# Performance work log

Measured on AMD Instinct MI355X. Metric: run time of the kernel, lower is better.

The kernel has to match this reference:

```python
import jax, jax.numpy as jnp
import numpy as np

VOCAB = 32000
H = 1024          # hidden_size + 8
I = 2 * H         # gru input size
SRC = 4096

def setup_inputs() -> dict:
    key = jax.random.key(0)
    ks = jax.random.split(key, 12)
    s = 0.02
    return {
        "word_input": jax.random.randint(ks[0], (1, 1), 0, VOCAB),
        "last_context": jax.random.normal(ks[1], (1, 1, H), jnp.float32),
        "prev_hidden": jax.random.normal(ks[2], (1, 1, H), jnp.float32),
        "encoder_outputs": jax.random.normal(ks[3], (SRC, 1, H), jnp.float32),
        "emb": jax.random.normal(ks[4], (VOCAB, H), jnp.float32) * s,
        "W_ih": jax.random.normal(ks[5], (3 * H, I), jnp.float32) * s,
        "W_hh": jax.random.normal(ks[6], (3 * H, H), jnp.float32) * s,
        "b_ih": jax.random.normal(ks[7], (3 * H,), jnp.float32) * s,
        "b_hh": jax.random.normal(ks[8], (3 * H,), jnp.float32) * s,
        "W_out": jax.random.normal(ks[9], (VOCAB, I), jnp.float32) * s,
        "b_out": jax.random.normal(ks[10], (VOCAB,), jnp.float32) * s,
    }

def reference(word_input, last_context, prev_hidden, encoder_outputs,
              emb, W_ih, W_hh, b_ih, b_hh, W_out, b_out):
    # embedding lookup (dropout is identity in eval)
    x = emb[word_input.reshape(-1)[0]]                # (H,)
    rnn_in = jnp.concatenate([x, last_context[0, 0]])  # (2H,)
    h = prev_hidden[0, 0]                              # (H,)

    # single-step GRU (PyTorch gate order: r, z, n)
    gi = W_ih @ rnn_in + b_ih                          # (3H,)
    gh = W_hh @ h + b_hh                               # (3H,)
    i_r, i_z, i_n = jnp.split(gi, 3)
    h_r, h_z, h_n = jnp.split(gh, 3)
    r = jax.nn.sigmoid(i_r + h_r)
    z = jax.nn.sigmoid(i_z + h_z)
    n = jnp.tanh(i_n + r * h_n)
    h_new = (1.0 - z) * n + z * h                      # (H,)
    current_hidden = h_new.reshape(1, 1, H)

    # Luong dot attention over encoder outputs
    enc = encoder_outputs[:, 0, :]                     # (S, H)
    scores = enc @ h_new                               # (S,)
    attn_weights = jax.nn.softmax(scores).reshape(1, 1, -1)
    attn_context = (attn_weights[0] @ enc).reshape(1, 1, H)

    joined = jnp.concatenate([h_new, attn_context[0, 0]])  # (2H,)
    logits = joined @ W_out.T + b_out                  # (vocab,)
    output = jax.nn.log_softmax(logits).reshape(1, -1)
    return (output, attn_context, current_hidden, attn_weights)
```

## Files before the change

### kernel.cpp

```cpp
#include <hip/hip_runtime.h>
#include <math.h>

#define H      1024
#define I2     2048
#define G3     3072
#define SRC    4096
#define VOCAB  32000

#define OUT_CTX   32000
#define OUT_HID   33024
#define OUT_ATTW  34048

#define WS_GI     0
#define WS_GH     3072
#define WS_HNEW   6144
#define WS_SCORES 7168
#define WS_ATTW   11264
#define WS_CTX    15360
#define WS_LOGITS 16384
#define WS_STATS  48384

__device__ __forceinline__ float wave_reduce_sum(float v) {
    #pragma unroll
    for (int off = 32; off > 0; off >>= 1)
        v += __shfl_down(v, off, 64);
    return v;
}

__device__ __forceinline__ float wave_reduce_max(float v) {
    #pragma unroll
    for (int off = 32; off > 0; off >>= 1)
        v = fmaxf(v, __shfl_down(v, off, 64));
    return v;
}

__global__ void gru_matvec_kernel(const int* __restrict__ word,
                                  const float* __restrict__ last_ctx,
                                  const float* __restrict__ prev_h,
                                  const float* __restrict__ emb,
                                  const float* __restrict__ W_ih,
                                  const float* __restrict__ W_hh,
                                  const float* __restrict__ b_ih,
                                  const float* __restrict__ b_hh,
                                  float* __restrict__ ws) {
    __shared__ float lds[8];
    const int j = blockIdx.x;
    const int tid = threadIdx.x;
    const int w = word[0];
    const float4* emb4 = (const float4*)(emb + (long)w * H);
    const float4* ctx4 = (const float4*)last_ctx;
    const float4* h4   = (const float4*)prev_h;

    const float4* Wi = (const float4*)(W_ih + (long)j * I2);
    float gi = 0.f;
    {
        float4 wv = Wi[tid];
        float4 xv = emb4[tid];
        gi += wv.x*xv.x + wv.y*xv.y + wv.z*xv.z + wv.w*xv.w;
        wv = Wi[tid + 256];
        xv = ctx4[tid];
        gi += wv.x*xv.x + wv.y*xv.y + wv.z*xv.z + wv.w*xv.w;
    }
    const float4* Wh = (const float4*)(W_hh + (long)j * H);
    float gh;
    {
        float4 wv = Wh[tid];
        float4 hv = h4[tid];
        gh = wv.x*hv.x + wv.y*hv.y + wv.z*hv.z + wv.w*hv.w;
    }

    const int lane = tid & 63, wid = tid >> 6;
    gi = wave_reduce_sum(gi);
    gh = wave_reduce_sum(gh);
    if (lane == 0) { lds[wid] = gi; lds[4 + wid] = gh; }
    __syncthreads();
    if (tid == 0) {
        float gis = lds[0] + lds[1] + lds[2] + lds[3];
        float ghs = lds[4] + lds[5] + lds[6] + lds[7];
        ws[WS_GI + j] = gis + b_ih[j];
        ws[WS_GH + j] = ghs + b_hh[j];
    }
}

__global__ void gru_gates_kernel(const float* __restrict__ prev_h,
                                 float* __restrict__ ws,
                                 float* __restrict__ out_hid) {
    const int j = threadIdx.x;
    const float ir = ws[WS_GI + j],        hr = ws[WS_GH + j];
    const float iz = ws[WS_GI + H + j],    hz = ws[WS_GH + H + j];
    const float in_ = ws[WS_GI + 2*H + j], hn = ws[WS_GH + 2*H + j];
    const float r = 1.f / (1.f + expf(-(ir + hr)));
    const float z = 1.f / (1.f + expf(-(iz + hz)));
    const float n = tanhf(in_ + r * hn);
    const float h = prev_h[j];
    const float hnew = (1.f - z) * n + z * h;
    ws[WS_HNEW + j] = hnew;
    out_hid[j] = hnew;
}

__global__ void attn_scores_kernel(const float* __restrict__ enc,
                                   const float* __restrict__ ws_in,
                                   float* __restrict__ ws) {
    __shared__ float lds[4];
    const int s = blockIdx.x, tid = threadIdx.x;
    float4 ev = ((const float4*)(enc + (long)s * H))[tid];
    float4 hv = ((const float4*)(ws_in + WS_HNEW))[tid];
    float d = ev.x*hv.x + ev.y*hv.y + ev.z*hv.z + ev.w*hv.w;
    const int lane = tid & 63, wid = tid >> 6;
    d = wave_reduce_sum(d);
    if (lane == 0) lds[wid] = d;
    __syncthreads();
    if (tid == 0) ws[WS_SCORES + s] = lds[0] + lds[1] + lds[2] + lds[3];
}

__global__ void attn_softmax_kernel(float* __restrict__ ws,
                                    float* __restrict__ out_attw) {
    __shared__ float lds[16];
    __shared__ float s_max, s_sum;
    const int tid = threadIdx.x;
    const int lane = tid & 63, wid = tid >> 6;
    float4 sv = ((const float4*)(ws + WS_SCORES))[tid];
    float m = fmaxf(fmaxf(sv.x, sv.y), fmaxf(sv.z, sv.w));
    m = wave_reduce_max(m);
    if (lane == 0) lds[wid] = m;
    __syncthreads();
    if (tid == 0) {
        float mm = lds[0];
        #pragma unroll
        for (int i = 1; i < 16; ++i) mm = fmaxf(mm, lds[i]);
        s_max = mm;
    }
    __syncthreads();
    const float mx = s_max;
    float4 e;
    e.x = expf(sv.x - mx); e.y = expf(sv.y - mx);
    e.z = expf(sv.z - mx); e.w = expf(sv.w - mx);
    float s = e.x + e.y + e.z + e.w;
    s = wave_reduce_sum(s);
    if (lane == 0) lds[wid] = s;
    __syncthreads();
    if (tid == 0) {
        float t = 0.f;
        #pragma unroll
        for (int i = 0; i < 16; ++i) t += lds[i];
        s_sum = t;
    }
    __syncthreads();
    const float inv = 1.f / s_sum;
    float4 o = make_float4(e.x*inv, e.y*inv, e.z*inv, e.w*inv);
    ((float4*)(ws + WS_ATTW))[tid] = o;
    ((float4*)out_attw)[tid] = o;
    ws[WS_CTX + tid] = 0.f;
}

__global__ void attn_context_kernel(const float* __restrict__ enc,
                                    float* __restrict__ ws) {
    const int tid = threadIdx.x;
    const int s0 = blockIdx.x * 128;
    float4 acc = make_float4(0.f, 0.f, 0.f, 0.f);
    for (int s = s0; s < s0 + 128; ++s) {
        const float wgt = ws[WS_ATTW + s];
        float4 ev = ((const float4*)(enc + (long)s * H))[tid];
        acc.x += wgt * ev.x; acc.y += wgt * ev.y;
        acc.z += wgt * ev.z; acc.w += wgt * ev.w;
    }
    float* ctx = ws + WS_CTX + tid * 4;
    atomicAdd(ctx + 0, acc.x); atomicAdd(ctx + 1, acc.y);
    atomicAdd(ctx + 2, acc.z); atomicAdd(ctx + 3, acc.w);
}

__global__ void out_proj_kernel(const float* __restrict__ W_out,
                                const float* __restrict__ b_out,
                                float* __restrict__ ws,
                                float* __restrict__ out_ctx) {
    const int tid = threadIdx.x;
    const int lane = tid & 63, wid = tid >> 6;
    const int v = blockIdx.x * 4 + wid;
    const float4* Wr = (const float4*)(W_out + (long)v * I2);
    const float4* h4 = (const float4*)(ws + WS_HNEW);
    const float4* c4 = (const float4*)(ws + WS_CTX);
    float acc = 0.f;
    #pragma unroll
    for (int r = 0; r < 8; ++r) {
        const int idx = lane + r * 64;
        float4 wv = Wr[idx];
        float4 jv = (r < 4) ? h4[idx] : c4[idx - 256];
        acc += wv.x*jv.x + wv.y*jv.y + wv.z*jv.z + wv.w*jv.w;
    }
    acc = wave_reduce_sum(acc);
    if (lane == 0) ws[WS_LOGITS + v] = acc + b_out[v];
    if (blockIdx.x == 0) {
        for (int k = tid; k < H; k += 256) out_ctx[k] = ws[WS_CTX + k];
    }
}

__global__ void lse_kernel(float* __restrict__ ws) {
    __shared__ float lds[16];
    __shared__ float s_max;
    const int tid = threadIdx.x;
    const int lane = tid & 63, wid = tid >> 6;
    const float* lg = ws + WS_LOGITS;
    float m = -INFINITY;
    for (int v = tid; v < VOCAB; v += 1024) m = fmaxf(m, lg[v]);
    m = wave_reduce_max(m);
    if (lane == 0) lds[wid] = m;
    __syncthreads();
    if (tid == 0) {
        float mm = lds[0];
        #pragma unroll
        for (int i = 1; i < 16; ++i) mm = fmaxf(mm, lds[i]);
        s_max = mm;
    }
    __syncthreads();
    const float mx = s_max;
    float s = 0.f;
    for (int v = tid; v < VOCAB; v += 1024) s += expf(lg[v] - mx);
    s = wave_reduce_sum(s);
    if (lane == 0) lds[wid] = s;
    __syncthreads();
    if (tid == 0) {
        float t = 0.f;
        #pragma unroll
        for (int i = 0; i < 16; ++i) t += lds[i];
        ws[WS_STATS] = mx + logf(t);
    }
}

__global__ void logsoftmax_write_kernel(const float* __restrict__ ws,
                                        float* __restrict__ out) {
    const int v = blockIdx.x * 256 + threadIdx.x;
    if (v < VOCAB) out[v] = ws[WS_LOGITS + v] - ws[WS_STATS];
}

extern "C" void kernel_launch(void* const* d_in, const int* in_sizes, int n_in,
                              void* d_out, int out_size, void* d_ws, size_t ws_size,
                              hipStream_t stream) {
    const int*   word     = (const int*)  d_in[0];
    const float* last_ctx = (const float*)d_in[1];
    const float* prev_h   = (const float*)d_in[2];
    const float* enc      = (const float*)d_in[3];
    const float* emb      = (const float*)d_in[4];
    const float* W_ih     = (const float*)d_in[5];
    const float* W_hh     = (const float*)d_in[6];
    const float* b_ih     = (const float*)d_in[7];
    const float* b_hh     = (const float*)d_in[8];
    const float* W_out    = (const float*)d_in[9];
    const float* b_out    = (const float*)d_in[10];
    float* out = (float*)d_out;
    float* ws  = (float*)d_ws;

    gru_matvec_kernel<<<G3, 256, 0, stream>>>(word, last_ctx, prev_h, emb,
                                              W_ih, W_hh, b_ih, b_hh, ws);
    gru_gates_kernel<<<1, 1024, 0, stream>>>(prev_h, ws, out + OUT_HID);
    attn_scores_kernel<<<SRC, 256, 0, stream>>>(enc, ws, ws);
    attn_softmax_kernel<<<1, 1024, 0, stream>>>(ws, out + OUT_ATTW);
    attn_context_kernel<<<32, 256, 0, stream>>>(enc, ws);
    out_proj_kernel<<<VOCAB / 4, 256, 0, stream>>>(W_out, b_out, ws, out + OUT_CTX);
    lse_kernel<<<1, 1024, 0, stream>>>(ws);
    logsoftmax_write_kernel<<<(VOCAB + 255) / 256, 256, 0, stream>>>(ws, out);
}
```

Baseline: 475.6 us.

## Fuse attention softmax into context kernel, add nontemporal weight loads, vectorize tails

Merges the single-block attention softmax into the context kernel. Each of 128 blocks recomputes the softmax statistics redundantly and weights its own 32-row slice of encoder outputs, and the context zeroing moves into the gate kernel. Weight matrices are streamed with nontemporal loads. The output projection now does 4 rows per wave, with the joined vector staged in LDS. The LSE and log-softmax write kernels use float4 accesses. This removes one launch and raises parallelism in the context reduction, at the cost of redundant softmax work in every block and more atomics.

```diff
diff --git a/kernel.cpp b/kernel.cpp
--- a/kernel.cpp
+++ b/kernel.cpp
@@ -15,7 +15,6 @@
 #define WS_GH     3072
 #define WS_HNEW   6144
 #define WS_SCORES 7168
-#define WS_ATTW   11264
 #define WS_CTX    15360
 #define WS_LOGITS 16384
 #define WS_STATS  48384
@@ -32,6 +31,13 @@
     for (int off = 32; off > 0; off >>= 1)
         v = fmaxf(v, __shfl_down(v, off, 64));
     return v;
+}
+
+typedef float vfloat4 __attribute__((ext_vector_type(4)));
+
+__device__ __forceinline__ float4 nt_load4(const float4* p) {
+    vfloat4 v = __builtin_nontemporal_load((const vfloat4*)p);
+    return make_float4(v.x, v.y, v.z, v.w);
 }
 
 __global__ void gru_matvec_kernel(const int* __restrict__ word,
@@ -54,17 +60,17 @@
     const float4* Wi = (const float4*)(W_ih + (long)j * I2);
     float gi = 0.f;
     {
-        float4 wv = Wi[tid];
+        float4 wv = nt_load4(&Wi[tid]);
         float4 xv = emb4[tid];
         gi += wv.x*xv.x + wv.y*xv.y + wv.z*xv.z + wv.w*xv.w;
-        wv = Wi[tid + 256];
+        wv = nt_load4(&Wi[tid + 256]);
         xv = ctx4[tid];
         gi += wv.x*xv.x + wv.y*xv.y + wv.z*xv.z + wv.w*xv.w;
     }
     const float4* Wh = (const float4*)(W_hh + (long)j * H);
     float gh;
     {
-        float4 wv = Wh[tid];
+        float4 wv = nt_load4(&Wh[tid]);
         float4 hv = h4[tid];
         gh = wv.x*hv.x + wv.y*hv.y + wv.z*hv.z + wv.w*hv.w;
     }
@@ -96,6 +102,7 @@
     const float hnew = (1.f - z) * n + z * h;
     ws[WS_HNEW + j] = hnew;
     out_hid[j] = hnew;
+    ws[WS_CTX + j] = 0.f;
 }
 
 __global__ void attn_scores_kernel(const float* __restrict__ enc,
@@ -113,53 +120,49 @@
     if (tid == 0) ws[WS_SCORES + s] = lds[0] + lds[1] + lds[2] + lds[3];
 }
 
-__global__ void attn_softmax_kernel(float* __restrict__ ws,
-                                    float* __restrict__ out_attw) {
-    __shared__ float lds[16];
-    __shared__ float s_max, s_sum;
-    const int tid = threadIdx.x;
-    const int lane = tid & 63, wid = tid >> 6;
-    float4 sv = ((const float4*)(ws + WS_SCORES))[tid];
-    float m = fmaxf(fmaxf(sv.x, sv.y), fmaxf(sv.z, sv.w));
+__global__ void attn_fused_kernel(const float* __restrict__ enc,
+                                  float* __restrict__ ws,
+                                  float* __restrict__ out_attw) {
+    __shared__ float s_e[SRC];
+    __shared__ float red[4];
+    __shared__ float s_stat;
+    const int tid = threadIdx.x;
+    const int lane = tid & 63, wid = tid >> 6;
+    const float4* sc4 = (const float4*)(ws + WS_SCORES);
+
+    float4 sv[4];
+    float m = -INFINITY;
+    #pragma unroll
+    for (int i = 0; i < 4; ++i) {
+        sv[i] = sc4[tid + 256 * i];
+        m = fmaxf(m, fmaxf(fmaxf(sv[i].x, sv[i].y), fmaxf(sv[i].z, sv[i].w)));
+    }
     m = wave_reduce_max(m);
-    if (lane == 0) lds[wid] = m;
-    __syncthreads();
-    if (tid == 0) {
-        float mm = lds[0];
-        #pragma unroll
-        for (int i = 1; i < 16; ++i) mm = fmaxf(mm, lds[i]);
-        s_max = mm;
-    }
-    __syncthreads();
-    const float mx = s_max;
-    float4 e;
-    e.x = expf(sv.x - mx); e.y = expf(sv.y - mx);
-    e.z = expf(sv.z - mx); e.w = expf(sv.w - mx);
-    float s = e.x + e.y + e.z + e.w;
-    s = wave_reduce_sum(s);
-    if (lane == 0) lds[wid] = s;
-    __syncthreads();
-    if (tid == 0) {
-        float t = 0.f;
-        #pragma unroll
-        for (int i = 0; i < 16; ++i) t += lds[i];
-        s_sum = t;
-    }
-    __syncthreads();
-    const float inv = 1.f / s_sum;
-    float4 o = make_float4(e.x*inv, e.y*inv, e.z*inv, e.w*inv);
-    ((float4*)(ws + WS_ATTW))[tid] = o;
-    ((float4*)out_attw)[tid] = o;
-    ws[WS_CTX + tid] = 0.f;
-}
-
-__global__ void attn_context_kernel(const float* __restrict__ enc,
-                                    float* __restrict__ ws) {
-    const int tid = threadIdx.x;
-    const int s0 = blockIdx.x * 128;
+    if (lane == 0) red[wid] = m;
+    __syncthreads();
+    if (tid == 0) s_stat = fmaxf(fmaxf(red[0], red[1]), fmaxf(red[2], red[3]));
+    __syncthreads();
+    const float mx = s_stat;
+    float sum = 0.f;
+    #pragma unroll
+    for (int i = 0; i < 4; ++i) {
+        float4 e;
+        e.x = expf(sv[i].x - mx); e.y = expf(sv[i].y - mx);
+        e.z = expf(sv[i].z - mx); e.w = expf(sv[i].w - mx);
+        ((float4*)s_e)[tid + 256 * i] = e;
+        sum += e.x + e.y + e.z + e.w;
+    }
+    sum = wave_reduce_sum(sum);
+    if (lane == 0) red[wid] = sum;
+    __syncthreads();
+    if (tid == 0) s_stat = red[0] + red[1] + red[2] + red[3];
+    __syncthreads();
+    const float inv = 1.f / s_stat;
+
+    const int s0 = blockIdx.x * 32;
     float4 acc = make_float4(0.f, 0.f, 0.f, 0.f);
-    for (int s = s0; s < s0 + 128; ++s) {
-        const float wgt = ws[WS_ATTW + s];
+    for (int s = s0; s < s0 + 32; ++s) {
+        const float wgt = s_e[s] * inv;
         float4 ev = ((const float4*)(enc + (long)s * H))[tid];
         acc.x += wgt * ev.x; acc.y += wgt * ev.y;
         acc.z += wgt * ev.z; acc.w += wgt * ev.w;
@@ -167,30 +170,45 @@
     float* ctx = ws + WS_CTX + tid * 4;
     atomicAdd(ctx + 0, acc.x); atomicAdd(ctx + 1, acc.y);
     atomicAdd(ctx + 2, acc.z); atomicAdd(ctx + 3, acc.w);
+
+    if (blockIdx.x == 0) {
+        #pragma unroll
+        for (int i = 0; i < 4; ++i) {
+            float4 e = ((float4*)s_e)[tid + 256 * i];
+            float4 o = make_float4(e.x * inv, e.y * inv, e.z * inv, e.w * inv);
+            ((float4*)out_attw)[tid + 256 * i] = o;
+        }
+    }
 }
 
 __global__ void out_proj_kernel(const float* __restrict__ W_out,
                                 const float* __restrict__ b_out,
                                 float* __restrict__ ws,
                                 float* __restrict__ out_ctx) {
-    const int tid = threadIdx.x;
-    const int lane = tid & 63, wid = tid >> 6;
-    const int v = blockIdx.x * 4 + wid;
-    const float4* Wr = (const float4*)(W_out + (long)v * I2);
-    const float4* h4 = (const float4*)(ws + WS_HNEW);
-    const float4* c4 = (const float4*)(ws + WS_CTX);
-    float acc = 0.f;
-    #pragma unroll
-    for (int r = 0; r < 8; ++r) {
-        const int idx = lane + r * 64;
-        float4 wv = Wr[idx];
-        float4 jv = (r < 4) ? h4[idx] : c4[idx - 256];
-        acc += wv.x*jv.x + wv.y*jv.y + wv.z*jv.z + wv.w*jv.w;
-    }
-    acc = wave_reduce_sum(acc);
-    if (lane == 0) ws[WS_LOGITS + v] = acc + b_out[v];
+    __shared__ float4 s_j[512];
+    const int tid = threadIdx.x;
+    const int lane = tid & 63, wid = tid >> 6;
+    s_j[tid]       = ((const float4*)(ws + WS_HNEW))[tid];
+    s_j[256 + tid] = ((const float4*)(ws + WS_CTX))[tid];
+    __syncthreads();
+
+    const int vbase = blockIdx.x * 16 + wid * 4;
+    #pragma unroll
+    for (int rr = 0; rr < 4; ++rr) {
+        const int v = vbase + rr;
+        const float4* Wr = (const float4*)(W_out + (long)v * I2);
+        float acc = 0.f;
+        #pragma unroll
+        for (int r = 0; r < 8; ++r) {
+            float4 wv = nt_load4(&Wr[lane + r * 64]);
+            float4 jv = s_j[lane + r * 64];
+            acc += wv.x*jv.x + wv.y*jv.y + wv.z*jv.z + wv.w*jv.w;
+        }
+        acc = wave_reduce_sum(acc);
+        if (lane == 0) ws[WS_LOGITS + v] = acc + b_out[v];
+    }
     if (blockIdx.x == 0) {
-        for (int k = tid; k < H; k += 256) out_ctx[k] = ws[WS_CTX + k];
+        ((float4*)out_ctx)[tid] = s_j[256 + tid];
     }
 }
 
@@ -199,9 +217,12 @@
     __shared__ float s_max;
     const int tid = threadIdx.x;
     const int lane = tid & 63, wid = tid >> 6;
-    const float* lg = ws + WS_LOGITS;
+    const float4* lg4 = (const float4*)(ws + WS_LOGITS);
     float m = -INFINITY;
-    for (int v = tid; v < VOCAB; v += 1024) m = fmaxf(m, lg[v]);
+    for (int i = tid; i < VOCAB / 4; i += 1024) {
+        float4 v = lg4[i];
+        m = fmaxf(m, fmaxf(fmaxf(v.x, v.y), fmaxf(v.z, v.w)));
+    }
     m = wave_reduce_max(m);
     if (lane == 0) lds[wid] = m;
     __syncthreads();
@@ -214,7 +235,10 @@
     __syncthreads();
     const float mx = s_max;
     float s = 0.f;
-    for (int v = tid; v < VOCAB; v += 1024) s += expf(lg[v] - mx);
+    for (int i = tid; i < VOCAB / 4; i += 1024) {
+        float4 v = lg4[i];
+        s += expf(v.x - mx) + expf(v.y - mx) + expf(v.z - mx) + expf(v.w - mx);
+    }
     s = wave_reduce_sum(s);
     if (lane == 0) lds[wid] = s;
     __syncthreads();
@@ -228,8 +252,13 @@
 
 __global__ void logsoftmax_write_kernel(const float* __restrict__ ws,
                                         float* __restrict__ out) {
-    const int v = blockIdx.x * 256 + threadIdx.x;
-    if (v < VOCAB) out[v] = ws[WS_LOGITS + v] - ws[WS_STATS];
+    const float lse = ws[WS_STATS];
+    const float4* lg4 = (const float4*)(ws + WS_LOGITS);
+    float4* out4 = (float4*)out;
+    for (int i = blockIdx.x * 256 + threadIdx.x; i < VOCAB / 4; i += gridDim.x * 256) {
+        float4 v = lg4[i];
+        out4[i] = make_float4(v.x - lse, v.y - lse, v.z - lse, v.w - lse);
+    }
 }
 
 extern "C" void kernel_launch(void* const* d_in, const int* in_sizes, int n_in,
@@ -253,9 +282,8 @@
                                               W_ih, W_hh, b_ih, b_hh, ws);
     gru_gates_kernel<<<1, 1024, 0, stream>>>(prev_h, ws, out + OUT_HID);
     attn_scores_kernel<<<SRC, 256, 0, stream>>>(enc, ws, ws);
-    attn_softmax_kernel<<<1, 1024, 0, stream>>>(ws, out + OUT_ATTW);
-    attn_context_kernel<<<32, 256, 0, stream>>>(enc, ws);
-    out_proj_kernel<<<VOCAB / 4, 256, 0, stream>>>(W_out, b_out, ws, out + OUT_CTX);
+    attn_fused_kernel<<<128, 256, 0, stream>>>(enc, ws, out + OUT_ATTW);
+    out_proj_kernel<<<VOCAB / 16, 256, 0, stream>>>(W_out, b_out, ws, out + OUT_CTX);
     lse_kernel<<<1, 1024, 0, stream>>>(ws);
-    logsoftmax_write_kernel<<<(VOCAB + 255) / 256, 256, 0, stream>>>(ws, out);
-}
+    logsoftmax_write_kernel<<<32, 256, 0, stream>>>(ws, out);
+}
```

Result: faster. 455.7 us (-4.2%).
